# Kernel optimization log

Measured on AMD Instinct MI355X. Metric: run time of the kernel, lower is better.

## Reference

```python
import math
import jax, jax.numpy as jnp
import numpy as np

B, H, HKV, L, S, D = 1, 32, 8, 2048, 2048, 128
N_REP = H // HKV          # 4
SCALE = 1.0 / math.sqrt(D)


def setup_inputs() -> dict:
    key = jax.random.key(0)
    k1, k2, k3, k4 = jax.random.split(key, 4)
    query = jax.random.normal(k1, (B, H, L, D), dtype=jnp.float32)
    k_ = jax.random.normal(k2, (B, HKV, S, D), dtype=jnp.float32)
    v_ = jax.random.normal(k3, (B, HKV, S, D), dtype=jnp.float32)
    attn_mask = jax.random.normal(k4, (B, 1, L, S), dtype=jnp.float32)
    return {"query": query, "key": k_, "value": v_, "attn_mask": attn_mask}


def reference(query, key, value, attn_mask):
    # repeat_kv: Q -> [B, HKV, n_rep, L, D]; K/V stay [B, HKV, S, D]
    # (the torch code reshapes K/V to [B, HKV, 1, S, D]; broadcasting via
    # einsum is equivalent), mask unsqueezed at dim 1 -> [B, 1, 1, L, S].
    q = query.reshape(B, HKV, N_REP, L, D)
    scores = jnp.einsum("bkrld,bksd->bkrls", q, key)          # [B,HKV,n_rep,L,S]
    scores = scores + attn_mask[:, None]                        # broadcast add
    # softmax_fp8(x, dim=-1, invAttnHead=1/sqrt(D)) scales input by invAttnHead
    w = jax.nn.softmax(scores * SCALE, axis=-1)
    # dropout_p = 0.0 -> identity
    out = jnp.einsum("bkrls,bksd->bkrld", w, value)             # [B,HKV,n_rep,L,D]
    return out
```

## Files before the change

kernel.cpp:

```cpp
#include <hip/hip_runtime.h>

#define NH   32
#define NKV  8
#define LQ   2048
#define SK   2048
#define DH   128
#define BM   128
#define BN   64
#define NT   (SK / BN)
#define VSTRIDE 72

typedef __attribute__((ext_vector_type(8)))  short bf8;
typedef __attribute__((ext_vector_type(16))) float f16v;
typedef __attribute__((ext_vector_type(4)))  unsigned int u32x4;

#define CL2E 0.12754308753f

#if __has_builtin(__builtin_amdgcn_exp2f)
#define EXP2F(x) __builtin_amdgcn_exp2f(x)
#else
#define EXP2F(x) exp2f(x)
#endif

__device__ __forceinline__ unsigned short f2bf(float f) {
    unsigned int u = __builtin_bit_cast(unsigned int, f);
    u = (u + 0x7FFFu + ((u >> 16) & 1u)) >> 16;
    return (unsigned short)u;
}

__device__ __forceinline__ unsigned int cvtpk_bf16(float lo, float hi) {
    unsigned int r;
    asm("v_cvt_pk_bf16_f32 %0, %1, %2" : "=v"(r) : "v"(lo), "v"(hi));
    return r;
}

__device__ __forceinline__ float bflo(unsigned int u) {
    return __builtin_bit_cast(float, u << 16);
}
__device__ __forceinline__ float bfhi(unsigned int u) {
    return __builtin_bit_cast(float, u & 0xFFFF0000u);
}

#define GLOAD_LDS16(g, l)                                                      \
    __builtin_amdgcn_global_load_lds(                                          \
        (const __attribute__((address_space(1))) void*)(g),                    \
        (__attribute__((address_space(3))) void*)(l), 16, 0, 0)

__global__ __launch_bounds__(256) void prep_kernel(
    const float* __restrict__ K, unsigned short* __restrict__ Kb,
    const float* __restrict__ V, unsigned short* __restrict__ VTb,
    const float* __restrict__ M, unsigned short* __restrict__ Mb)
{
    __shared__ __align__(16) unsigned short Vl[DH * VSTRIDE];
    const int tid = threadIdx.x;
    const int bid = blockIdx.x;

    if (bid < 1024) {
        unsigned int cid = bid * 256 + tid;
        unsigned int p   = cid & 15;
        unsigned int row = cid >> 4;
        unsigned int s   = row & (SK - 1);
        unsigned int c   = p ^ (s & 15);
        const float* src = K + (size_t)row * DH + c * 8;
        float4 a = *(const float4*)(src);
        float4 b = *(const float4*)(src + 4);
        bf8 o;
        o[0] = (short)f2bf(a.x); o[1] = (short)f2bf(a.y);
        o[2] = (short)f2bf(a.z); o[3] = (short)f2bf(a.w);
        o[4] = (short)f2bf(b.x); o[5] = (short)f2bf(b.y);
        o[6] = (short)f2bf(b.z); o[7] = (short)f2bf(b.w);
        *(bf8*)(Kb + (size_t)row * DH + p * 8) = o;
    } else if (bid < 1280) {
        const int vb = bid - 1024;
        const int kv = vb >> 5;
        const int t  = vb & 31;
        const int s0 = t * 64;
        const float* Vh = V + (size_t)kv * SK * DH;
        #pragma unroll
        for (int i = 0; i < 8; ++i) {
            int idx = tid * 4 + i * 1024;
            int s = idx >> 7, d = idx & 127;
            const float4 v4 = *(const float4*)(Vh + (size_t)(s0 + s) * DH + d);
            Vl[(d + 0) * VSTRIDE + s] = f2bf(v4.x);
            Vl[(d + 1) * VSTRIDE + s] = f2bf(v4.y);
            Vl[(d + 2) * VSTRIDE + s] = f2bf(v4.z);
            Vl[(d + 3) * VSTRIDE + s] = f2bf(v4.w);
        }
        __syncthreads();
        unsigned short* out = VTb + (size_t)(kv * 32 + t) * (DH * 64);
        #pragma unroll
        for (int i = 0; i < 4; ++i) {
            int c = tid + i * 256;
            int d = c >> 3, p = c & 7;
            int sc = (p ^ (d & 7)) * 8;
            *(bf8*)(out + d * 64 + p * 8) = *(const bf8*)(Vl + d * VSTRIDE + sc);
        }
    } else {
        unsigned int cid = (bid - 1280) * 256 + tid;
        unsigned int row = cid >> 8;
        unsigned int l   = (cid & 255) * 8;
        unsigned int T   = l & ~63u;
        unsigned int loc = l & 63;
        unsigned int mt = loc >> 5, w = loc & 31;
        unsigned int hh = w >> 4, g0 = (w >> 2) & 3;
        const float* src = M + (size_t)row * SK + T + mt * 32 + hh * 4;
        float4 a = *(const float4*)(src + g0 * 8);
        float4 b = *(const float4*)(src + (g0 + 1) * 8);
        bf8 o;
        o[0] = (short)f2bf(a.x * CL2E); o[1] = (short)f2bf(a.y * CL2E);
        o[2] = (short)f2bf(a.z * CL2E); o[3] = (short)f2bf(a.w * CL2E);
        o[4] = (short)f2bf(b.x * CL2E); o[5] = (short)f2bf(b.y * CL2E);
        o[6] = (short)f2bf(b.z * CL2E); o[7] = (short)f2bf(b.w * CL2E);
        *(bf8*)(Mb + (size_t)row * SK + l) = o;
    }
}

#define QKSPLIT(BASE, SNX)                                                     \
    {                                                                          \
      f16v tL, tH;                                                             \
      _Pragma("unroll")                                                        \
      for (int r = 0; r < 16; ++r) { tL[r] = 0.f; tH[r] = 0.f; }               \
      __builtin_amdgcn_s_setprio(1);                                           \
      _Pragma("unroll")                                                        \
      for (int ks = 0; ks < 4; ++ks) {                                         \
        bf8 aKl = *(const bf8*)((BASE) + (krow0 ^ (ks << 5)));                 \
        bf8 aKh = *(const bf8*)((BASE) + (krow0 ^ ((ks + 4) << 5)));           \
        tL = __builtin_amdgcn_mfma_f32_32x32x16_bf16(aKl, bQ[ks], tL, 0, 0, 0);\
        tH = __builtin_amdgcn_mfma_f32_32x32x16_bf16(aKh, bQ[ks + 4], tH, 0, 0, 0);\
      }                                                                        \
      __builtin_amdgcn_s_setprio(0);                                           \
      _Pragma("unroll")                                                        \
      for (int r = 0; r < 16; ++r) SNX[r] = tL[r] + tH[r];                     \
    }

#define BODY(T, CUR, SC0, SC1, SN0, SN1)                                       \
  {                                                                            \
    __syncthreads();                                                           \
    const unsigned short* mp = Mq + (T) * 64;                                  \
    u32x4 mA0 = *(const u32x4*)(mp);                                           \
    u32x4 mB0 = *(const u32x4*)(mp + 8);                                       \
    u32x4 mA1 = *(const u32x4*)(mp + 32);                                      \
    u32x4 mB1 = *(const u32x4*)(mp + 40);                                      \
    {                                                                          \
      const int tv = ((T) + 1) & (NT - 1);                                     \
      const int tk = ((T) + 2) & (NT - 1);                                     \
      const unsigned char* vsrc = Vg + (size_t)tv * 16384 + stoff;             \
      const unsigned char* ksrc = Kg + (size_t)tk * 16384 + stoff;             \
      unsigned char* vdst = VB + ((CUR) ^ 1) * 16384 + stoff;                  \
      unsigned char* kdst = KB + (CUR) * 16384 + stoff;                        \
      _Pragma("unroll")                                                        \
      for (int c = 0; c < 4; ++c) GLOAD_LDS16(vsrc + c * 1024, vdst + c * 1024); \
      _Pragma("unroll")                                                        \
      for (int c = 0; c < 4; ++c) GLOAD_LDS16(ksrc + c * 1024, kdst + c * 1024); \
    }                                                                          \
    __builtin_amdgcn_sched_barrier(0);                                         \
    const unsigned char* kbn = KB + ((CUR) ^ 1) * 16384;                       \
    const unsigned char* vbc = VB + (CUR) * 16384;                             \
    QKSPLIT(kbn, SN0)                                                          \
    unsigned int pk0[8], pk1[8];                                               \
    _Pragma("unroll")                                                          \
    for (int g = 0; g < 4; ++g) {                                              \
      unsigned int u0 = (g < 2) ? mA0[g * 2 + 0] : mB0[(g - 2) * 2 + 0];       \
      unsigned int u1 = (g < 2) ? mA0[g * 2 + 1] : mB0[(g - 2) * 2 + 1];       \
      float e0 = EXP2F(fmaf(SC0[g*4+0], CL2E, bflo(u0)));                      \
      float e1 = EXP2F(fmaf(SC0[g*4+1], CL2E, bfhi(u0)));                      \
      float e2 = EXP2F(fmaf(SC0[g*4+2], CL2E, bflo(u1)));                      \
      float e3 = EXP2F(fmaf(SC0[g*4+3], CL2E, bfhi(u1)));                      \
      lpA += (e0 + e1) + (e2 + e3);                                            \
      pk0[g*2+0] = cvtpk_bf16(e0, e1);                                         \
      pk0[g*2+1] = cvtpk_bf16(e2, e3);                                         \
    }                                                                          \
    QKSPLIT(kbn + 8192, SN1)                                                   \
    _Pragma("unroll")                                                          \
    for (int g = 0; g < 4; ++g) {                                              \
      unsigned int u0 = (g < 2) ? mA1[g * 2 + 0] : mB1[(g - 2) * 2 + 0];       \
      unsigned int u1 = (g < 2) ? mA1[g * 2 + 1] : mB1[(g - 2) * 2 + 1];       \
      float e0 = EXP2F(fmaf(SC1[g*4+0], CL2E, bflo(u0)));                      \
      float e1 = EXP2F(fmaf(SC1[g*4+1], CL2E, bfhi(u0)));                      \
      float e2 = EXP2F(fmaf(SC1[g*4+2], CL2E, bflo(u1)));                      \
      float e3 = EXP2F(fmaf(SC1[g*4+3], CL2E, bfhi(u1)));                      \
      lpB += (e0 + e1) + (e2 + e3);                                            \
      pk1[g*2+0] = cvtpk_bf16(e0, e1);                                         \
      pk1[g*2+1] = cvtpk_bf16(e2, e3);                                         \
    }                                                                          \
    bf8 bP[4];                                                                 \
    _Pragma("unroll")                                                          \
    for (int ks = 0; ks < 4; ++ks) {                                           \
      unsigned int* pk = (ks >> 1) ? pk1 : pk0;                                \
      const int kk = ks & 1;                                                   \
      unsigned int a0 = pk[kk*4+0], b0 = pk[kk*4+2];                           \
      unsigned int a1 = pk[kk*4+1], b1 = pk[kk*4+3];                           \
      asm volatile("v_permlane32_swap_b32 %0, %1" : "+v"(a0), "+v"(b0));       \
      asm volatile("v_permlane32_swap_b32 %0, %1" : "+v"(a1), "+v"(b1));       \
      u32x4 w; w[0] = a0; w[1] = a1; w[2] = b0; w[3] = b1;                     \
      bP[ks] = __builtin_bit_cast(bf8, w);                                     \
    }                                                                          \
    __builtin_amdgcn_s_setprio(1);                                             \
    _Pragma("unroll")                                                          \
    for (int dt = 0; dt < 4; ++dt) {                                           \
      _Pragma("unroll")                                                        \
      for (int ks = 0; ks < 4; ++ks) {                                         \
        bf8 aV = *(const bf8*)(vbc + dt * 4096 + (vrowz ^ (ks << 5)));         \
        accO[dt] = __builtin_amdgcn_mfma_f32_32x32x16_bf16(aV, bP[ks], accO[dt], 0, 0, 0); \
      }                                                                        \
    }                                                                          \
    __builtin_amdgcn_s_setprio(0);                                             \
  }

__global__ __launch_bounds__(256, 2) void fattn_kernel(
    const float* __restrict__ Q, const unsigned short* __restrict__ Kb,
    const unsigned short* __restrict__ VTb, const unsigned short* __restrict__ Mb,
    float* __restrict__ O)
{
    __shared__ __align__(1024) unsigned char smem[65536];
    unsigned char* KB = smem;
    unsigned char* VB = smem + 32768;

    const int tid  = threadIdx.x;
    const int wave = tid >> 6;
    const int lane = tid & 63;
    const int l32  = lane & 31;
    const int hh   = lane >> 5;

    const int bx = ((int)blockIdx.x & 7) * 64 + ((int)blockIdx.x >> 3);
    const int h  = bx >> 4;
    const int lt = bx & 15;
    const int q0 = lt * BM;
    const int kv = h >> 2;

    const float* Qh = Q + (size_t)h * LQ * DH;
    const unsigned char* Kg = (const unsigned char*)(Kb  + (size_t)kv * SK * DH);
    const unsigned char* Vg = (const unsigned char*)(VTb + (size_t)kv * SK * DH);

    const int qrow = q0 + wave * 32 + l32;
    const unsigned short* Mq = Mb + (size_t)qrow * SK + hh * 16;

    bf8 bQ[8];
    {
        const float* qp = Qh + (size_t)qrow * DH + hh * 8;
        #pragma unroll
        for (int ks = 0; ks < 8; ++ks) {
            float4 a = *(const float4*)(qp + ks * 16);
            float4 b = *(const float4*)(qp + ks * 16 + 4);
            bf8 o;
            o[0] = (short)f2bf(a.x); o[1] = (short)f2bf(a.y);
            o[2] = (short)f2bf(a.z); o[3] = (short)f2bf(a.w);
            o[4] = (short)f2bf(b.x); o[5] = (short)f2bf(b.y);
            o[6] = (short)f2bf(b.z); o[7] = (short)f2bf(b.w);
            bQ[ks] = o;
        }
    }

    const int krow0 = l32 * 256 + ((hh * 16) ^ ((l32 & 15) << 4));
    const int vrowz = l32 * 128 + ((hh * 16) ^ ((l32 & 7) << 4));

    const int stoff = wave * 4096 + lane * 16;

    f16v accO[4];
    #pragma unroll
    for (int dt = 0; dt < 4; ++dt)
        #pragma unroll
        for (int r = 0; r < 16; ++r) accO[dt][r] = 0.f;
    float lpA = 0.f, lpB = 0.f;

    #pragma unroll
    for (int c = 0; c < 4; ++c) GLOAD_LDS16(Kg + stoff + c * 1024, KB + stoff + c * 1024);
    #pragma unroll
    for (int c = 0; c < 4; ++c) GLOAD_LDS16(Vg + stoff + c * 1024, VB + stoff + c * 1024);
    #pragma unroll
    for (int c = 0; c < 4; ++c) GLOAD_LDS16(Kg + 16384 + stoff + c * 1024, KB + 16384 + stoff + c * 1024);
    __syncthreads();

    f16v sA0, sA1, sB0, sB1;
    QKSPLIT(KB, sA0)
    QKSPLIT(KB + 8192, sA1)

    for (int tt = 0; tt < NT; tt += 2) {
        BODY(tt + 0, 0, sA0, sA1, sB0, sB1)
        BODY(tt + 1, 1, sB0, sB1, sA0, sA1)
    }

    asm volatile("s_waitcnt vmcnt(0)" ::: "memory");
    float lpart = lpA + lpB;
    float l = lpart + __shfl_xor(lpart, 32);
    float inv = 1.0f / l;
    float* Op = O + (size_t)h * LQ * DH + (size_t)qrow * DH;
    #pragma unroll
    for (int dt = 0; dt < 4; ++dt) {
        #pragma unroll
        for (int g = 0; g < 4; ++g) {
            int d = dt * 32 + g * 8 + hh * 4;
            float4 o;
            o.x = accO[dt][g * 4 + 0] * inv;
            o.y = accO[dt][g * 4 + 1] * inv;
            o.z = accO[dt][g * 4 + 2] * inv;
            o.w = accO[dt][g * 4 + 3] * inv;
            *(float4*)(Op + d) = o;
        }
    }
}

extern "C" void kernel_launch(void* const* d_in, const int* in_sizes, int n_in,
                              void* d_out, int out_size, void* d_ws, size_t ws_size,
                              hipStream_t stream) {
    const float* Q = (const float*)d_in[0];
    const float* K = (const float*)d_in[1];
    const float* V = (const float*)d_in[2];
    const float* M = (const float*)d_in[3];
    float* O = (float*)d_out;

    unsigned short* Kb  = (unsigned short*)d_ws;
    unsigned short* VTb = Kb + (size_t)NKV * SK * DH;
    unsigned short* Mb  = VTb + (size_t)NKV * DH * SK;

    prep_kernel<<<dim3(3328), 256, 0, stream>>>(K, Kb, V, VTb, M, Mb);

    dim3 grid(NH * (LQ / BM));
    fattn_kernel<<<grid, 256, 0, stream>>>(Q, Kb, VTb, Mb, O);
}
```

Before: 183.5 us.

## Double block to 8 waves and stagger QK and softmax-PV phases across wave halves

```diff
diff --git a/kernel.cpp b/kernel.cpp
--- a/kernel.cpp
+++ b/kernel.cpp
@@ -5,7 +5,7 @@
 #define LQ   2048
 #define SK   2048
 #define DH   128
-#define BM   128
+#define BM   256
 #define BN   64
 #define NT   (SK / BN)
 #define VSTRIDE 72
@@ -115,22 +115,71 @@
     }
 }
 
-#define QKSPLIT(BASE, SNX)                                                     \
+#define QKM(KBASE, SN0, SN1)                                                   \
+    _Pragma("unroll")                                                          \
+    for (int r = 0; r < 16; ++r) { SN0[r] = 0.f; SN1[r] = 0.f; }               \
+    __builtin_amdgcn_s_setprio(1);                                             \
+    _Pragma("unroll")                                                          \
+    for (int ks = 0; ks < 8; ++ks) {                                           \
+      bf8 aK = *(const bf8*)((KBASE) + (krow0 ^ (ks << 5)));                   \
+      SN0 = __builtin_amdgcn_mfma_f32_32x32x16_bf16(aK, bQ[ks], SN0, 0, 0, 0); \
+    }                                                                          \
+    _Pragma("unroll")                                                          \
+    for (int ks = 0; ks < 8; ++ks) {                                           \
+      bf8 aK = *(const bf8*)((KBASE) + 8192 + (krow0 ^ (ks << 5)));            \
+      SN1 = __builtin_amdgcn_mfma_f32_32x32x16_bf16(aK, bQ[ks], SN1, 0, 0, 0); \
+    }                                                                          \
+    __builtin_amdgcn_s_setprio(0);
+
+#define SMPV(SC0, SC1)                                                         \
     {                                                                          \
-      f16v tL, tH;                                                             \
+      unsigned int pk0[8], pk1[8];                                             \
       _Pragma("unroll")                                                        \
-      for (int r = 0; r < 16; ++r) { tL[r] = 0.f; tH[r] = 0.f; }               \
+      for (int g = 0; g < 4; ++g) {                                            \
+        unsigned int u0 = (g < 2) ? mA0[g * 2 + 0] : mB0[(g - 2) * 2 + 0];     \
+        unsigned int u1 = (g < 2) ? mA0[g * 2 + 1] : mB0[(g - 2) * 2 + 1];     \
+        float e0 = EXP2F(fmaf(SC0[g*4+0], CL2E, bflo(u0)));                    \
+        float e1 = EXP2F(fmaf(SC0[g*4+1], CL2E, bfhi(u0)));                    \
+        float e2 = EXP2F(fmaf(SC0[g*4+2], CL2E, bflo(u1)));                    \
+        float e3 = EXP2F(fmaf(SC0[g*4+3], CL2E, bfhi(u1)));                    \
+        lpA += (e0 + e1) + (e2 + e3);                                          \
+        pk0[g*2+0] = cvtpk_bf16(e0, e1);                                       \
+        pk0[g*2+1] = cvtpk_bf16(e2, e3);                                       \
+      }                                                                        \
+      _Pragma("unroll")                                                        \
+      for (int g = 0; g < 4; ++g) {                                            \
+        unsigned int u0 = (g < 2) ? mA1[g * 2 + 0] : mB1[(g - 2) * 2 + 0];     \
+        unsigned int u1 = (g < 2) ? mA1[g * 2 + 1] : mB1[(g - 2) * 2 + 1];     \
+        float e0 = EXP2F(fmaf(SC1[g*4+0], CL2E, bflo(u0)));                    \
+        float e1 = EXP2F(fmaf(SC1[g*4+1], CL2E, bfhi(u0)));                    \
+        float e2 = EXP2F(fmaf(SC1[g*4+2], CL2E, bflo(u1)));                    \
+        float e3 = EXP2F(fmaf(SC1[g*4+3], CL2E, bfhi(u1)));                    \
+        lpB += (e0 + e1) + (e2 + e3);                                          \
+        pk1[g*2+0] = cvtpk_bf16(e0, e1);                                       \
+        pk1[g*2+1] = cvtpk_bf16(e2, e3);                                       \
+      }                                                                        \
+      bf8 bP[4];                                                               \
+      _Pragma("unroll")                                                        \
+      for (int ks = 0; ks < 4; ++ks) {                                         \
+        unsigned int* pk = (ks >> 1) ? pk1 : pk0;                              \
+        const int kk = ks & 1;                                                 \
+        unsigned int a0 = pk[kk*4+0], b0 = pk[kk*4+2];                         \
+        unsigned int a1 = pk[kk*4+1], b1 = pk[kk*4+3];                         \
+        asm volatile("v_permlane32_swap_b32 %0, %1" : "+v"(a0), "+v"(b0));     \
+        asm volatile("v_permlane32_swap_b32 %0, %1" : "+v"(a1), "+v"(b1));     \
+        u32x4 w; w[0] = a0; w[1] = a1; w[2] = b0; w[3] = b1;                   \
+        bP[ks] = __builtin_bit_cast(bf8, w);                                   \
+      }                                                                        \
       __builtin_amdgcn_s_setprio(1);                                           \
       _Pragma("unroll")                                                        \
-      for (int ks = 0; ks < 4; ++ks) {                                         \
-        bf8 aKl = *(const bf8*)((BASE) + (krow0 ^ (ks << 5)));                 \
-        bf8 aKh = *(const bf8*)((BASE) + (krow0 ^ ((ks + 4) << 5)));           \
-        tL = __builtin_amdgcn_mfma_f32_32x32x16_bf16(aKl, bQ[ks], tL, 0, 0, 0);\
-        tH = __builtin_amdgcn_mfma_f32_32x32x16_bf16(aKh, bQ[ks + 4], tH, 0, 0, 0);\
+      for (int dt = 0; dt < 4; ++dt) {                                         \
+        _Pragma("unroll")                                                      \
+        for (int ks = 0; ks < 4; ++ks) {                                       \
+          bf8 aV = *(const bf8*)(vbc + dt * 4096 + (vrowz ^ (ks << 5)));       \
+          accO[dt] = __builtin_amdgcn_mfma_f32_32x32x16_bf16(aV, bP[ks], accO[dt], 0, 0, 0); \
+        }                                                                      \
       }                                                                        \
       __builtin_amdgcn_s_setprio(0);                                           \
-      _Pragma("unroll")                                                        \
-      for (int r = 0; r < 16; ++r) SNX[r] = tL[r] + tH[r];                     \
     }
 
 #define BODY(T, CUR, SC0, SC1, SN0, SN1)                                       \
@@ -148,66 +197,24 @@
       const unsigned char* ksrc = Kg + (size_t)tk * 16384 + stoff;             \
       unsigned char* vdst = VB + ((CUR) ^ 1) * 16384 + stoff;                  \
       unsigned char* kdst = KB + (CUR) * 16384 + stoff;                        \
-      _Pragma("unroll")                                                        \
-      for (int c = 0; c < 4; ++c) GLOAD_LDS16(vsrc + c * 1024, vdst + c * 1024); \
-      _Pragma("unroll")                                                        \
-      for (int c = 0; c < 4; ++c) GLOAD_LDS16(ksrc + c * 1024, kdst + c * 1024); \
+      GLOAD_LDS16(vsrc, vdst);                                                 \
+      GLOAD_LDS16(vsrc + 8192, vdst + 8192);                                   \
+      GLOAD_LDS16(ksrc, kdst);                                                 \
+      GLOAD_LDS16(ksrc + 8192, kdst + 8192);                                   \
     }                                                                          \
     __builtin_amdgcn_sched_barrier(0);                                         \
     const unsigned char* kbn = KB + ((CUR) ^ 1) * 16384;                       \
     const unsigned char* vbc = VB + (CUR) * 16384;                             \
-    QKSPLIT(kbn, SN0)                                                          \
-    unsigned int pk0[8], pk1[8];                                               \
-    _Pragma("unroll")                                                          \
-    for (int g = 0; g < 4; ++g) {                                              \
-      unsigned int u0 = (g < 2) ? mA0[g * 2 + 0] : mB0[(g - 2) * 2 + 0];       \
-      unsigned int u1 = (g < 2) ? mA0[g * 2 + 1] : mB0[(g - 2) * 2 + 1];       \
-      float e0 = EXP2F(fmaf(SC0[g*4+0], CL2E, bflo(u0)));                      \
-      float e1 = EXP2F(fmaf(SC0[g*4+1], CL2E, bfhi(u0)));                      \
-      float e2 = EXP2F(fmaf(SC0[g*4+2], CL2E, bflo(u1)));                      \
-      float e3 = EXP2F(fmaf(SC0[g*4+3], CL2E, bfhi(u1)));                      \
-      lpA += (e0 + e1) + (e2 + e3);                                            \
-      pk0[g*2+0] = cvtpk_bf16(e0, e1);                                         \
-      pk0[g*2+1] = cvtpk_bf16(e2, e3);                                         \
+    if (wave < 4) {                                                            \
+      QKM(kbn, SN0, SN1)                                                       \
+      SMPV(SC0, SC1)                                                           \
+    } else {                                                                   \
+      SMPV(SC0, SC1)                                                           \
+      QKM(kbn, SN0, SN1)                                                       \
     }                                                                          \
-    QKSPLIT(kbn + 8192, SN1)                                                   \
-    _Pragma("unroll")                                                          \
-    for (int g = 0; g < 4; ++g) {                                              \
-      unsigned int u0 = (g < 2) ? mA1[g * 2 + 0] : mB1[(g - 2) * 2 + 0];       \
-      unsigned int u1 = (g < 2) ? mA1[g * 2 + 1] : mB1[(g - 2) * 2 + 1];       \
-      float e0 = EXP2F(fmaf(SC1[g*4+0], CL2E, bflo(u0)));                      \
-      float e1 = EXP2F(fmaf(SC1[g*4+1], CL2E, bfhi(u0)));                      \
-      float e2 = EXP2F(fmaf(SC1[g*4+2], CL2E, bflo(u1)));                      \
-      float e3 = EXP2F(fmaf(SC1[g*4+3], CL2E, bfhi(u1)));                      \
-      lpB += (e0 + e1) + (e2 + e3);                                            \
-      pk1[g*2+0] = cvtpk_bf16(e0, e1);                                         \
-      pk1[g*2+1] = cvtpk_bf16(e2, e3);                                         \
-    }                                                                          \
-    bf8 bP[4];                                                                 \
-    _Pragma("unroll")                                                          \
-    for (int ks = 0; ks < 4; ++ks) {                                           \
-      unsigned int* pk = (ks >> 1) ? pk1 : pk0;                                \
-      const int kk = ks & 1;                                                   \
-      unsigned int a0 = pk[kk*4+0], b0 = pk[kk*4+2];                           \
-      unsigned int a1 = pk[kk*4+1], b1 = pk[kk*4+3];                           \
-      asm volatile("v_permlane32_swap_b32 %0, %1" : "+v"(a0), "+v"(b0));       \
-      asm volatile("v_permlane32_swap_b32 %0, %1" : "+v"(a1), "+v"(b1));       \
-      u32x4 w; w[0] = a0; w[1] = a1; w[2] = b0; w[3] = b1;                     \
-      bP[ks] = __builtin_bit_cast(bf8, w);                                     \
-    }                                                                          \
-    __builtin_amdgcn_s_setprio(1);                                             \
-    _Pragma("unroll")                                                          \
-    for (int dt = 0; dt < 4; ++dt) {                                           \
-      _Pragma("unroll")                                                        \
-      for (int ks = 0; ks < 4; ++ks) {                                         \
-        bf8 aV = *(const bf8*)(vbc + dt * 4096 + (vrowz ^ (ks << 5)));         \
-        accO[dt] = __builtin_amdgcn_mfma_f32_32x32x16_bf16(aV, bP[ks], accO[dt], 0, 0, 0); \
-      }                                                                        \
-    }                                                                          \
-    __builtin_amdgcn_s_setprio(0);                                             \
   }
 
-__global__ __launch_bounds__(256, 2) void fattn_kernel(
+__global__ __launch_bounds__(512, 2) void fattn_kernel(
     const float* __restrict__ Q, const unsigned short* __restrict__ Kb,
     const unsigned short* __restrict__ VTb, const unsigned short* __restrict__ Mb,
     float* __restrict__ O)
@@ -222,9 +229,9 @@
     const int l32  = lane & 31;
     const int hh   = lane >> 5;
 
-    const int bx = ((int)blockIdx.x & 7) * 64 + ((int)blockIdx.x >> 3);
-    const int h  = bx >> 4;
-    const int lt = bx & 15;
+    const int bx = ((int)blockIdx.x & 7) * 32 + ((int)blockIdx.x >> 3);
+    const int h  = bx >> 3;
+    const int lt = bx & 7;
     const int q0 = lt * BM;
     const int kv = h >> 2;
 
@@ -254,7 +261,7 @@
     const int krow0 = l32 * 256 + ((hh * 16) ^ ((l32 & 15) << 4));
     const int vrowz = l32 * 128 + ((hh * 16) ^ ((l32 & 7) << 4));
 
-    const int stoff = wave * 4096 + lane * 16;
+    const int stoff = tid * 16;
 
     f16v accO[4];
     #pragma unroll
@@ -263,17 +270,16 @@
         for (int r = 0; r < 16; ++r) accO[dt][r] = 0.f;
     float lpA = 0.f, lpB = 0.f;
 
-    #pragma unroll
-    for (int c = 0; c < 4; ++c) GLOAD_LDS16(Kg + stoff + c * 1024, KB + stoff + c * 1024);
-    #pragma unroll
-    for (int c = 0; c < 4; ++c) GLOAD_LDS16(Vg + stoff + c * 1024, VB + stoff + c * 1024);
-    #pragma unroll
-    for (int c = 0; c < 4; ++c) GLOAD_LDS16(Kg + 16384 + stoff + c * 1024, KB + 16384 + stoff + c * 1024);
+    GLOAD_LDS16(Kg + stoff, KB + stoff);
+    GLOAD_LDS16(Kg + stoff + 8192, KB + stoff + 8192);
+    GLOAD_LDS16(Vg + stoff, VB + stoff);
+    GLOAD_LDS16(Vg + stoff + 8192, VB + stoff + 8192);
+    GLOAD_LDS16(Kg + 16384 + stoff, KB + 16384 + stoff);
+    GLOAD_LDS16(Kg + 24576 + stoff, KB + 24576 + stoff);
     __syncthreads();
 
     f16v sA0, sA1, sB0, sB1;
-    QKSPLIT(KB, sA0)
-    QKSPLIT(KB + 8192, sA1)
+    QKM(KB, sA0, sA1)
 
     for (int tt = 0; tt < NT; tt += 2) {
         BODY(tt + 0, 0, sA0, sA1, sB0, sB1)
@@ -316,5 +322,5 @@
     prep_kernel<<<dim3(3328), 256, 0, stream>>>(K, Kb, V, VTb, M, Mb);
 
     dim3 grid(NH * (LQ / BM));
-    fattn_kernel<<<grid, 256, 0, stream>>>(Q, Kb, VTb, Mb, O);
-}
+    fattn_kernel<<<grid, 512, 0, stream>>>(Q, Kb, VTb, Mb, O);
+}
```

After: 194.9 us. 6.2% more time.
